# Optimization experiments

Measured on AMD Instinct MI355X. Metric: run time of the kernel, lower is better.

The kernel has to match this reference:

```python
import jax, jax.numpy as jnp
import numpy as np
import math

B, N, DIM = 2, 4096, 1024
H, D, M = 16, 64, 256


def setup_inputs() -> dict:
    key = jax.random.key(0)
    ks = jax.random.split(key, 6)
    s = 1.0 / math.sqrt(DIM)
    return {
        "x": jax.random.normal(ks[0], (B, N, DIM), dtype=jnp.float32),
        "w_q": jax.random.normal(ks[1], (DIM, H * D), dtype=jnp.float32) * s,
        "w_k": jax.random.normal(ks[2], (DIM, H * D), dtype=jnp.float32) * s,
        "w_v": jax.random.normal(ks[3], (DIM, H * D), dtype=jnp.float32) * s,
        "w_o": jax.random.normal(ks[4], (H * D, DIM), dtype=jnp.float32) * s,
        "b_o": jnp.zeros((DIM,), dtype=jnp.float32),
        "omega": jax.random.normal(ks[5], (M, D), dtype=jnp.float32),
    }


def _heads(t):
    # [B, N, H*D] -> [B, H, N, D]
    return t.reshape(B, N, H, D).transpose(0, 2, 1, 3)


def _phi(t, omega):
    # t: [B,H,N,D], omega: [M,D] -> [B,H,N,M]
    proj = jnp.einsum("bhnd,md->bhnm", t, omega)
    norm = 0.5 * jnp.sum(t * t, axis=-1, keepdims=True)
    return jnp.exp(proj - norm) / math.sqrt(M)


def reference(x, w_q, w_k, w_v, w_o, b_o, omega):
    q = _heads(x @ w_q)
    k = _heads(x @ w_k)
    v = _heads(x @ w_v)
    phi_q = _phi(q, omega)          # [B,H,N,M]
    phi_k = _phi(k, omega)          # [B,H,N,M]
    kv = jnp.einsum("bhnm,bhnd->bhmd", phi_k, v)   # [B,H,M,D]
    k_sum = phi_k.sum(axis=2)                       # [B,H,M]
    z = 1.0 / (jnp.einsum("bhnm,bhm->bhn", phi_q, k_sum) + 1e-6)
    out = jnp.einsum("bhnm,bhmd->bhnd", phi_q, kv) * z[..., None]
    out = out.transpose(0, 2, 1, 3).reshape(B, N, H * D)
    return out @ w_o + b_o
```

## Files before the change

kernel.cpp:

```cpp
#include <hip/hip_runtime.h>

#define DEVI __device__ __forceinline__

using f32x4 = __attribute__((ext_vector_type(4))) float;
using fvec4 = __attribute__((ext_vector_type(4))) float;
using s16x4 = __attribute__((ext_vector_type(4))) short;
using s16x8 = __attribute__((ext_vector_type(8))) short;

DEVI unsigned short f2bf_rn(float f) {
  union { float f; unsigned u; } v; v.f = f;
  unsigned r = v.u + 0x7fffu + ((v.u >> 16) & 1u);
  return (unsigned short)(r >> 16);
}
DEVI float bf2f(unsigned short h) {
  union { unsigned u; float f; } v; v.u = ((unsigned)h) << 16;
  return v.f;
}
DEVI f32x4 mfma16(s16x8 a, s16x8 b, f32x4 c) {
  return __builtin_amdgcn_mfma_f32_16x16x32_bf16(a, b, c, 0, 0, 0);
}
DEVI void gld16(const void* g, void* lds) {
  __builtin_amdgcn_global_load_lds(
      (const __attribute__((address_space(1))) unsigned int*)g,
      (__attribute__((address_space(3))) unsigned int*)lds, 16, 0, 0);
}

__global__ __launch_bounds__(256) void k_split_x(
    const float* __restrict__ X,
    unsigned short* __restrict__ XH, unsigned short* __restrict__ XL)
{
  size_t i = ((size_t)blockIdx.x * 256 + threadIdx.x) * 8;
  fvec4 a = *(const fvec4*)&X[i];
  fvec4 b = *(const fvec4*)&X[i + 4];
  s16x8 hv, lv;
#pragma unroll
  for (int j = 0; j < 4; ++j) {
    unsigned short h = f2bf_rn(a[j]);
    hv[j] = (short)h; lv[j] = (short)f2bf_rn(a[j] - bf2f(h));
  }
#pragma unroll
  for (int j = 0; j < 4; ++j) {
    unsigned short h = f2bf_rn(b[j]);
    hv[4 + j] = (short)h; lv[4 + j] = (short)f2bf_rn(b[j] - bf2f(h));
  }
  *(s16x8*)&XH[i] = hv;
  *(s16x8*)&XL[i] = lv;
}

__global__ __launch_bounds__(256) void k_prep_w(
    const float* __restrict__ wq, const float* __restrict__ wk,
    const float* __restrict__ wv, const float* __restrict__ wo,
    const float* __restrict__ omega,
    unsigned short* __restrict__ WTh, unsigned short* __restrict__ WOT,
    unsigned short* __restrict__ OMB)
{
  __shared__ float tile[64][65];
  const int z = blockIdx.z;
  const int t = threadIdx.x;
  if (z == 4) {
    int bid = blockIdx.x * 16 + blockIdx.y;
    if (bid < 16) {
      int i = (bid * 256 + t) * 4;
      fvec4 v = *(const fvec4*)&omega[i];
      s16x4 hv;
#pragma unroll
      for (int q = 0; q < 4; ++q) hv[q] = (short)f2bf_rn(v[q]);
      *(s16x4*)&OMB[i] = hv;
    }
    return;
  }
  const float* src = (z == 0) ? wq : (z == 1) ? wk : (z == 2) ? wv : wo;
  const int k0 = blockIdx.x * 64;
  const int n0 = blockIdx.y * 64;
#pragma unroll
  for (int j = 0; j < 4; ++j) {
    int r = (t >> 4) + 16 * j;
    int c = (t & 15) * 4;
    fvec4 v = *(const fvec4*)&src[(size_t)(k0 + r) * 1024 + n0 + c];
#pragma unroll
    for (int i = 0; i < 4; ++i) tile[r][c + i] = v[i];
  }
  __syncthreads();
#pragma unroll
  for (int j = 0; j < 4; ++j) {
    int n = (t >> 4) + 16 * j;
    int kc = (t & 15) * 4;
    s16x4 hv;
#pragma unroll
    for (int i = 0; i < 4; ++i) hv[i] = (short)f2bf_rn(tile[kc + i][n]);
    if (z < 3) {
      *(s16x4*)&WTh[(size_t)(z * 1024 + n0 + n) * 1024 + k0 + kc] = hv;
    } else {
      *(s16x4*)&WOT[(size_t)(n0 + n) * 1024 + k0 + kc] = hv;
    }
  }
}

__global__ __launch_bounds__(256) void k_gemm_qkv(
    const unsigned short* __restrict__ XH, const unsigned short* __restrict__ XL,
    const unsigned short* __restrict__ WTh,
    unsigned short* __restrict__ QH, unsigned short* __restrict__ QL,
    unsigned short* __restrict__ KH, unsigned short* __restrict__ KL,
    unsigned short* __restrict__ VB)
{
  __shared__ unsigned short AH[2][128 * 32];
  __shared__ unsigned short BHs[2][128 * 32];
  __shared__ unsigned short AL[2][128 * 32];
  const int flat = blockIdx.y * 24 + blockIdx.x;
  const int swz = (flat & 7) * 192 + (flat >> 3);
  const int cb = swz % 24;
  const int rb = swz / 24;
  const int t = threadIdx.x;
  const int w = t >> 6, l = t & 63;
  const bool tp = (cb < 16);
  f32x4 acc[4][4];
#pragma unroll
  for (int a = 0; a < 4; ++a)
#pragma unroll
    for (int b = 0; b < 4; ++b) acc[a][b] = (f32x4)0.f;

  const int r0 = w * 32;
  const int lrow = l >> 2;
  const int lcol = (l & 3) * 8;
  const size_t gA = (size_t)(rb * 128 + r0 + lrow) * 1024 + lcol;
  const size_t gB = (size_t)(cb * 128 + r0 + lrow) * 1024 + lcol;
  const int lds0 = r0 * 32;
  const int lds1 = (r0 + 16) * 32;

  const int wm = (w & 1) * 64, wn = (w >> 1) * 64;
  const int lr = l & 15, ko = (l >> 4) * 8;

  auto STAGE = [&](int buf, int k0) {
    gld16(&XH[gA + k0], &AH[buf][lds0]);
    gld16(&XH[gA + (size_t)16 * 1024 + k0], &AH[buf][lds1]);
    if (tp) {
      gld16(&XL[gA + k0], &AL[buf][lds0]);
      gld16(&XL[gA + (size_t)16 * 1024 + k0], &AL[buf][lds1]);
    }
    gld16(&WTh[gB + k0], &BHs[buf][lds0]);
    gld16(&WTh[gB + (size_t)16 * 1024 + k0], &BHs[buf][lds1]);
  };

  STAGE(0, 0);
  int cur = 0;
  for (int ks = 0; ks < 32; ++ks) {
    if (ks < 31) {
      STAGE(cur ^ 1, (ks + 1) * 32);
      if (tp) asm volatile("s_waitcnt vmcnt(6)" ::: "memory");
      else    asm volatile("s_waitcnt vmcnt(4)" ::: "memory");
    } else {
      asm volatile("s_waitcnt vmcnt(0)" ::: "memory");
    }
    __builtin_amdgcn_s_barrier();
    asm volatile("" ::: "memory");
    s16x8 ah[4], al[4], bh[4];
#pragma unroll
    for (int f = 0; f < 4; ++f) {
      ah[f] = *(const s16x8*)&AH[cur][(wm + f * 16 + lr) * 32 + ko];
      bh[f] = *(const s16x8*)&BHs[cur][(wn + f * 16 + lr) * 32 + ko];
    }
    if (tp) {
#pragma unroll
      for (int f = 0; f < 4; ++f) al[f] = *(const s16x8*)&AL[cur][(wm + f * 16 + lr) * 32 + ko];
    }
#pragma unroll
    for (int fa = 0; fa < 4; ++fa)
#pragma unroll
      for (int fb = 0; fb < 4; ++fb) {
        acc[fa][fb] = mfma16(ah[fa], bh[fb], acc[fa][fb]);
        if (tp) acc[fa][fb] = mfma16(al[fa], bh[fb], acc[fa][fb]);
      }
    asm volatile("s_waitcnt lgkmcnt(0)" ::: "memory");
    __builtin_amdgcn_s_barrier();
    asm volatile("" ::: "memory");
    cur ^= 1;
  }
  const int lg = l >> 4;
#pragma unroll
  for (int fa = 0; fa < 4; ++fa)
#pragma unroll
    for (int r = 0; r < 4; ++r) {
      int row = rb * 128 + wm + fa * 16 + lg * 4 + r;
#pragma unroll
      for (int fb = 0; fb < 4; ++fb) {
        int col = cb * 128 + wn + fb * 16 + lr;
        float v = acc[fa][fb][r];
        if (tp) {
          unsigned short hs = f2bf_rn(v);
          unsigned short ls = f2bf_rn(v - bf2f(hs));
          if (cb < 8) {
            QH[(size_t)row * 1024 + col] = hs;
            QL[(size_t)row * 1024 + col] = ls;
          } else {
            KH[(size_t)row * 1024 + col - 1024] = hs;
            KL[(size_t)row * 1024 + col - 1024] = ls;
          }
        } else {
          VB[(size_t)row * 1024 + col - 2048] = f2bf_rn(v);
        }
      }
    }
}

__global__ __launch_bounds__(512, 1) void k_phik_kv(
    const unsigned short* __restrict__ KH, const unsigned short* __restrict__ KL,
    const unsigned short* __restrict__ VB,
    const unsigned short* __restrict__ OMB, float* __restrict__ KVP)
{
  __shared__ unsigned short KHs[64][72], KLs[64][72];
  __shared__ unsigned short PKT[256][72];
  __shared__ unsigned short AVT[80][72];
  __shared__ float norm_s[64];
  const int nc = blockIdx.x;
  const int bh = blockIdx.y;
  const int b = bh >> 4, h = bh & 15;
  const int t = threadIdx.x, w = t >> 6, l = t & 63;
  const int lr = l & 15, lg = l >> 4, ko8 = lg * 8;

  s16x8 omf[2][2];
#pragma unroll
  for (int ksub = 0; ksub < 2; ++ksub)
#pragma unroll
    for (int f = 0; f < 2; ++f)
      omf[ksub][f] = *(const s16x8*)&OMB[(w * 32 + f * 16 + lr) * 64 + ksub * 32 + ko8];

  for (int e = t; e < 16 * 64; e += 512) {
    int rr = e >> 6, cc = e & 63;
    AVT[64 + rr][cc] = (rr == 0) ? (unsigned short)0x3F80 : (unsigned short)0;
  }

  f32x4 acc2[5][2];
#pragma unroll
  for (int a = 0; a < 5; ++a)
#pragma unroll
    for (int bb = 0; bb < 2; ++bb) acc2[a][bb] = (f32x4)0.f;

  for (int st = 0; st < 8; ++st) {
    const int n0 = nc * 512 + st * 64;
    __syncthreads();
    {
      int r = t >> 3, c8 = (t & 7) * 8;
      size_t o = (size_t)(b * 4096 + n0 + r) * 1024 + h * 64 + c8;
      s16x8 vh = *(const s16x8*)&KH[o];
      s16x8 vl = *(const s16x8*)&KL[o];
      *(s16x8*)&KHs[r][c8] = vh;
      *(s16x8*)&KLs[r][c8] = vl;
      float ss = 0.f;
#pragma unroll
      for (int i = 0; i < 8; ++i) {
        float q = bf2f((unsigned short)vh[i]) + bf2f((unsigned short)vl[i]);
        ss += q * q;
      }
      ss += __shfl_xor(ss, 1);
      ss += __shfl_xor(ss, 2);
      ss += __shfl_xor(ss, 4);
      if ((t & 7) == 0) norm_s[r] = 0.5f * ss;
    }
    {
      int n = t >> 3, dq = (t & 7) * 8;
      s16x8 v = *(const s16x8*)&VB[(size_t)(b * 4096 + n0 + n) * 1024 + h * 64 + dq];
#pragma unroll
      for (int i = 0; i < 8; ++i) AVT[dq + i][n] = (unsigned short)v[i];
    }
    __syncthreads();
    f32x4 acc[4][2];
#pragma unroll
    for (int a = 0; a < 4; ++a)
#pragma unroll
      for (int bb = 0; bb < 2; ++bb) acc[a][bb] = (f32x4)0.f;
#pragma unroll
    for (int ksub = 0; ksub < 2; ++ksub) {
      int ko = ksub * 32 + ko8;
      s16x8 ah[4], al[4];
#pragma unroll
      for (int f = 0; f < 4; ++f) {
        ah[f] = *(const s16x8*)&KHs[f * 16 + lr][ko];
        al[f] = *(const s16x8*)&KLs[f * 16 + lr][ko];
      }
#pragma unroll
      for (int fa = 0; fa < 4; ++fa)
#pragma unroll
        for (int fb = 0; fb < 2; ++fb) {
          acc[fa][fb] = mfma16(ah[fa], omf[ksub][fb], acc[fa][fb]);
          acc[fa][fb] = mfma16(al[fa], omf[ksub][fb], acc[fa][fb]);
        }
    }
#pragma unroll
    for (int fa = 0; fa < 4; ++fa)
#pragma unroll
      for (int r = 0; r < 4; ++r) {
        int n = fa * 16 + lg * 4 + r;
        float nm = norm_s[n];
#pragma unroll
        for (int fb = 0; fb < 2; ++fb) {
          int m = w * 32 + fb * 16 + lr;
          float p = __expf(acc[fa][fb][r] - nm) * 0.0625f;
          PKT[m][n] = f2bf_rn(p);
        }
      }
    __syncthreads();
#pragma unroll
    for (int ksub = 0; ksub < 2; ++ksub) {
      int ko = ksub * 32 + ko8;
      s16x8 fA[5], fB[2];
#pragma unroll
      for (int f = 0; f < 5; ++f) fA[f] = *(const s16x8*)&AVT[f * 16 + lr][ko];
#pragma unroll
      for (int f = 0; f < 2; ++f) fB[f] = *(const s16x8*)&PKT[w * 32 + f * 16 + lr][ko];
#pragma unroll
      for (int fa = 0; fa < 5; ++fa)
#pragma unroll
        for (int fb = 0; fb < 2; ++fb) acc2[fa][fb] = mfma16(fA[fa], fB[fb], acc2[fa][fb]);
    }
  }
#pragma unroll
  for (int fa = 0; fa < 5; ++fa)
#pragma unroll
    for (int r = 0; r < 4; ++r) {
      int dp = fa * 16 + lg * 4 + r;
#pragma unroll
      for (int fb = 0; fb < 2; ++fb) {
        int m = w * 32 + fb * 16 + lr;
        KVP[(size_t)((bh * 8 + nc) * 80 + dp) * 256 + m] = acc2[fa][fb][r];
      }
    }
}

__global__ __launch_bounds__(256) void k_kv_reduce(
    const float* __restrict__ KVP, unsigned short* __restrict__ KVTB)
{
  int idx = blockIdx.x * 256 + threadIdx.x;
  if (idx >= 32 * 80 * 256) return;
  int bh = idx / (80 * 256);
  int rem = idx % (80 * 256);
  float s = 0.f;
#pragma unroll
  for (int nci = 0; nci < 8; ++nci) s += KVP[(size_t)(bh * 8 + nci) * 80 * 256 + rem];
  KVTB[idx] = f2bf_rn(s);
}

__global__ __launch_bounds__(256) void k_phiq_attn(
    const unsigned short* QH, const unsigned short* QL,
    const unsigned short* __restrict__ OMB,
    const unsigned short* __restrict__ KVTB,
    unsigned short* ATT)
{
  __shared__ unsigned short QHs[64][72], QLs[64][72];
  __shared__ unsigned short PQ[64][264];
  __shared__ float norm_s[64];
  const int nt = blockIdx.x;
  const int bh = blockIdx.y;
  const int t = threadIdx.x, w = t >> 6, l = t & 63;
  const int b = bh >> 4, h = bh & 15;
  const int lr = l & 15, lg = l >> 4, ko8 = lg * 8;

  s16x8 omf[2][4];
#pragma unroll
  for (int ksub = 0; ksub < 2; ++ksub)
#pragma unroll
    for (int f = 0; f < 4; ++f)
      omf[ksub][f] = *(const s16x8*)&OMB[(w * 64 + f * 16 + lr) * 64 + ksub * 32 + ko8];

  {
    int r = t >> 2, cq = (t & 3) * 4;
    float ss = 0.f;
#pragma unroll
    for (int j = 0; j < 4; ++j) {
      int c = cq + 16 * j;
      size_t o = (size_t)(b * 4096 + nt * 64 + r) * 1024 + h * 64 + c;
      s16x4 vh = *(const s16x4*)&QH[o];
      s16x4 vl = *(const s16x4*)&QL[o];
      *(s16x4*)&QHs[r][c] = vh;
      *(s16x4*)&QLs[r][c] = vl;
#pragma unroll
      for (int i = 0; i < 4; ++i) {
        float q = bf2f((unsigned short)vh[i]) + bf2f((unsigned short)vl[i]);
        ss += q * q;
      }
    }
    ss += __shfl_xor(ss, 1);
    ss += __shfl_xor(ss, 2);
    if ((t & 3) == 0) norm_s[r] = 0.5f * ss;
  }
  __syncthreads();
  f32x4 acc[4][4];
#pragma unroll
  for (int a = 0; a < 4; ++a)
#pragma unroll
    for (int bb = 0; bb < 4; ++bb) acc[a][bb] = (f32x4)0.f;
#pragma unroll
  for (int ksub = 0; ksub < 2; ++ksub) {
    int ko = ksub * 32 + ko8;
    s16x8 ah[4], al[4];
#pragma unroll
    for (int f = 0; f < 4; ++f) {
      ah[f] = *(const s16x8*)&QHs[f * 16 + lr][ko];
      al[f] = *(const s16x8*)&QLs[f * 16 + lr][ko];
    }
#pragma unroll
    for (int fa = 0; fa < 4; ++fa)
#pragma unroll
      for (int fb = 0; fb < 4; ++fb) {
        acc[fa][fb] = mfma16(ah[fa], omf[ksub][fb], acc[fa][fb]);
        acc[fa][fb] = mfma16(al[fa], omf[ksub][fb], acc[fa][fb]);
      }
  }
#pragma unroll
  for (int fa = 0; fa < 4; ++fa)
#pragma unroll
    for (int r = 0; r < 4; ++r) {
      int n = fa * 16 + lg * 4 + r;
      float nm = norm_s[n];
#pragma unroll
      for (int fb = 0; fb < 4; ++fb) {
        int m = w * 64 + fb * 16 + lr;
        float p = __expf(acc[fa][fb][r] - nm) * 0.0625f;
        PQ[n][m] = f2bf_rn(p);
      }
    }
  __syncthreads();
  const size_t kvbase = (size_t)bh * 80 * 256;
  f32x4 acc2[5];
#pragma unroll
  for (int bb = 0; bb < 5; ++bb) acc2[bb] = (f32x4)0.f;
  for (int ks = 0; ks < 8; ++ks) {
    const int m0 = ks * 32;
    s16x8 fA = *(const s16x8*)&PQ[w * 16 + lr][m0 + ko8];
    s16x8 fB[5];
#pragma unroll
    for (int f = 0; f < 5; ++f)
      fB[f] = *(const s16x8*)&KVTB[kvbase + (size_t)(f * 16 + lr) * 256 + m0 + ko8];
#pragma unroll
    for (int fb = 0; fb < 5; ++fb) acc2[fb] = mfma16(fA, fB[fb], acc2[fb]);
  }
#pragma unroll
  for (int r = 0; r < 4; ++r) {
    float den = __shfl(acc2[4][r], (l & 48));
    float z = 1.f / (den + 1e-6f);
    int n = nt * 64 + w * 16 + lg * 4 + r;
#pragma unroll
    for (int fb = 0; fb < 4; ++fb) {
      int col = h * 64 + fb * 16 + lr;
      ATT[(size_t)(b * 4096 + n) * 1024 + col] = f2bf_rn(acc2[fb][r] * z);
    }
  }
}

__global__ __launch_bounds__(256) void k_gemm_out(
    const unsigned short* __restrict__ ATT,
    const unsigned short* __restrict__ WOT,
    const float* __restrict__ b_o,
    float* __restrict__ OUT)
{
  __shared__ unsigned short As[3][128 * 32], Bs[3][128 * 32];
  const int flat = blockIdx.y * 8 + blockIdx.x;
  const int swz = (flat & 7) * 64 + (flat >> 3);
  const int cb = swz % 8;
  const int rb = swz / 8;
  const int t = threadIdx.x, w = t >> 6, l = t & 63;
  f32x4 acc[4][4];
#pragma unroll
  for (int a = 0; a < 4; ++a)
#pragma unroll
    for (int bb = 0; bb < 4; ++bb) acc[a][bb] = (f32x4)0.f;

  const int r0 = w * 32;
  const int lrow = l >> 2;
  const int lcol = (l & 3) * 8;
  const size_t gA = (size_t)(rb * 128 + r0 + lrow) * 1024 + lcol;
  const size_t gB = (size_t)(cb * 128 + r0 + lrow) * 1024 + lcol;
  const int lds0 = r0 * 32;
  const int lds1 = (r0 + 16) * 32;

  const int wm = (w & 1) * 64, wn = (w >> 1) * 64;
  const int lr = l & 15, ko = (l >> 4) * 8;

  auto STAGE = [&](int buf, int k0) {
    gld16(&ATT[gA + k0], &As[buf][lds0]);
    gld16(&ATT[gA + (size_t)16 * 1024 + k0], &As[buf][lds1]);
    gld16(&WOT[gB + k0], &Bs[buf][lds0]);
    gld16(&WOT[gB + (size_t)16 * 1024 + k0], &Bs[buf][lds1]);
  };

  STAGE(0, 0);
  STAGE(1, 32);
  int cur = 0;
  for (int ks = 0; ks < 32; ++ks) {
    if (ks < 30) {
      int nxt = (cur >= 1) ? cur - 1 : 2;
      STAGE(nxt, (ks + 2) * 32);
      asm volatile("s_waitcnt vmcnt(8)" ::: "memory");
    } else if (ks == 30) {
      asm volatile("s_waitcnt vmcnt(4)" ::: "memory");
    } else {
      asm volatile("s_waitcnt vmcnt(0)" ::: "memory");
    }
    __builtin_amdgcn_s_barrier();
    asm volatile("" ::: "memory");
    s16x8 fA[4], fB[4];
#pragma unroll
    for (int f = 0; f < 4; ++f) {
      fA[f] = *(const s16x8*)&As[cur][(wm + f * 16 + lr) * 32 + ko];
      fB[f] = *(const s16x8*)&Bs[cur][(wn + f * 16 + lr) * 32 + ko];
    }
#pragma unroll
    for (int fa = 0; fa < 4; ++fa)
#pragma unroll
      for (int fb = 0; fb < 4; ++fb) acc[fa][fb] = mfma16(fA[fa], fB[fb], acc[fa][fb]);
    asm volatile("s_waitcnt lgkmcnt(0)" ::: "memory");
    __builtin_amdgcn_s_barrier();
    asm volatile("" ::: "memory");
    cur = (cur < 2) ? cur + 1 : 0;
  }
  const int lg = l >> 4;
#pragma unroll
  for (int fa = 0; fa < 4; ++fa)
#pragma unroll
    for (int r = 0; r < 4; ++r) {
      int row = rb * 128 + wm + fa * 16 + lg * 4 + r;
#pragma unroll
      for (int fb = 0; fb < 4; ++fb) {
        int col = cb * 128 + wn + fb * 16 + lr;
        OUT[(size_t)row * 1024 + col] = acc[fa][fb][r] + b_o[col];
      }
    }
}

extern "C" void kernel_launch(void* const* d_in, const int* in_sizes, int n_in,
                              void* d_out, int out_size, void* d_ws, size_t ws_size,
                              hipStream_t stream)
{
  const float* x  = (const float*)d_in[0];
  const float* wq = (const float*)d_in[1];
  const float* wk = (const float*)d_in[2];
  const float* wv = (const float*)d_in[3];
  const float* wo = (const float*)d_in[4];
  const float* bo = (const float*)d_in[5];
  const float* om = (const float*)d_in[6];
  float* out = (float*)d_out;

  const size_t PLANE = (size_t)8192 * 1024 * 2;
  char* ws = (char*)d_ws;
  unsigned short* WOT = (unsigned short*)(ws);
  char* segB = ws + 2097152;
  char* segC = segB + 2 * PLANE;
  char* segD = segC + 4 * PLANE;
  char* segE = segD + 26214400;

  unsigned short* QH  = (unsigned short*)segB;
  unsigned short* QL  = (unsigned short*)(segB + PLANE);
  unsigned short* ATT = (unsigned short*)segB;

  unsigned short* KH  = (unsigned short*)segC;
  unsigned short* KL  = (unsigned short*)(segC + PLANE);
  unsigned short* VB  = (unsigned short*)(segC + 2 * PLANE);
  unsigned short* XH  = (unsigned short*)(segC + 3 * PLANE);

  unsigned short* WTh = (unsigned short*)segD;
  unsigned short* XL  = (unsigned short*)(segD + 6291456);
  float* KVP = (float*)segD;
  unsigned short* KVTB = (unsigned short*)segE;
  unsigned short* OMB  = (unsigned short*)(segE + 1310720);

  k_split_x<<<dim3(4096), 256, 0, stream>>>(x, XH, XL);
  k_prep_w<<<dim3(16, 16, 5), 256, 0, stream>>>(wq, wk, wv, wo, om, WTh, WOT, OMB);
  k_gemm_qkv<<<dim3(24, 64), 256, 0, stream>>>(XH, XL, WTh, QH, QL, KH, KL, VB);
  k_phik_kv<<<dim3(8, 32), 512, 0, stream>>>(KH, KL, VB, OMB, KVP);
  k_kv_reduce<<<dim3(2560), 256, 0, stream>>>(KVP, KVTB);
  k_phiq_attn<<<dim3(64, 32), 256, 0, stream>>>(QH, QL, OMB, KVTB, ATT);
  k_gemm_out<<<dim3(8, 64), 256, 0, stream>>>(ATT, WOT, bo, out);
}
```

Before: 228.2 us.

## Load GEMM B fragments directly from global into registers, bypassing LDS

```diff
diff --git a/kernel.cpp b/kernel.cpp
--- a/kernel.cpp
+++ b/kernel.cpp
@@ -104,7 +104,6 @@
     unsigned short* __restrict__ VB)
 {
   __shared__ unsigned short AH[2][128 * 32];
-  __shared__ unsigned short BHs[2][128 * 32];
   __shared__ unsigned short AL[2][128 * 32];
   const int flat = blockIdx.y * 24 + blockIdx.x;
   const int swz = (flat & 7) * 192 + (flat >> 3);
@@ -123,12 +122,16 @@
   const int lrow = l >> 2;
   const int lcol = (l & 3) * 8;
   const size_t gA = (size_t)(rb * 128 + r0 + lrow) * 1024 + lcol;
-  const size_t gB = (size_t)(cb * 128 + r0 + lrow) * 1024 + lcol;
   const int lds0 = r0 * 32;
   const int lds1 = (r0 + 16) * 32;
 
   const int wm = (w & 1) * 64, wn = (w >> 1) * 64;
   const int lr = l & 15, ko = (l >> 4) * 8;
+
+  const unsigned short* Bp[4];
+#pragma unroll
+  for (int f = 0; f < 4; ++f)
+    Bp[f] = &WTh[(size_t)(cb * 128 + wn + f * 16 + lr) * 1024 + ko];
 
   auto STAGE = [&](int buf, int k0) {
     gld16(&XH[gA + k0], &AH[buf][lds0]);
@@ -137,32 +140,33 @@
       gld16(&XL[gA + k0], &AL[buf][lds0]);
       gld16(&XL[gA + (size_t)16 * 1024 + k0], &AL[buf][lds1]);
     }
-    gld16(&WTh[gB + k0], &BHs[buf][lds0]);
-    gld16(&WTh[gB + (size_t)16 * 1024 + k0], &BHs[buf][lds1]);
   };
 
   STAGE(0, 0);
   int cur = 0;
   for (int ks = 0; ks < 32; ++ks) {
+    const int k0 = ks * 32;
+    s16x8 bh[4];
+#pragma unroll
+    for (int f = 0; f < 4; ++f) bh[f] = *(const s16x8*)(Bp[f] + k0);
+    asm volatile("" ::: "memory");
     if (ks < 31) {
-      STAGE(cur ^ 1, (ks + 1) * 32);
-      if (tp) asm volatile("s_waitcnt vmcnt(6)" ::: "memory");
-      else    asm volatile("s_waitcnt vmcnt(4)" ::: "memory");
+      STAGE(cur ^ 1, k0 + 32);
+      if (tp) asm volatile("s_waitcnt vmcnt(8)" ::: "memory");
+      else    asm volatile("s_waitcnt vmcnt(6)" ::: "memory");
     } else {
-      asm volatile("s_waitcnt vmcnt(0)" ::: "memory");
+      asm volatile("s_waitcnt vmcnt(4)" ::: "memory");
     }
     __builtin_amdgcn_s_barrier();
     asm volatile("" ::: "memory");
-    s16x8 ah[4], al[4], bh[4];
-#pragma unroll
-    for (int f = 0; f < 4; ++f) {
-      ah[f] = *(const s16x8*)&AH[cur][(wm + f * 16 + lr) * 32 + ko];
-      bh[f] = *(const s16x8*)&BHs[cur][(wn + f * 16 + lr) * 32 + ko];
-    }
+    s16x8 ah[4], al[4];
+#pragma unroll
+    for (int f = 0; f < 4; ++f) ah[f] = *(const s16x8*)&AH[cur][(wm + f * 16 + lr) * 32 + ko];
     if (tp) {
 #pragma unroll
       for (int f = 0; f < 4; ++f) al[f] = *(const s16x8*)&AL[cur][(wm + f * 16 + lr) * 32 + ko];
     }
+    __builtin_amdgcn_s_setprio(1);
 #pragma unroll
     for (int fa = 0; fa < 4; ++fa)
 #pragma unroll
@@ -170,6 +174,7 @@
         acc[fa][fb] = mfma16(ah[fa], bh[fb], acc[fa][fb]);
         if (tp) acc[fa][fb] = mfma16(al[fa], bh[fb], acc[fa][fb]);
       }
+    __builtin_amdgcn_s_setprio(0);
     asm volatile("s_waitcnt lgkmcnt(0)" ::: "memory");
     __builtin_amdgcn_s_barrier();
     asm volatile("" ::: "memory");
@@ -452,7 +457,7 @@
     const float* __restrict__ b_o,
     float* __restrict__ OUT)
 {
-  __shared__ unsigned short As[3][128 * 32], Bs[3][128 * 32];
+  __shared__ unsigned short As[2][128 * 32];
   const int flat = blockIdx.y * 8 + blockIdx.x;
   const int swz = (flat & 7) * 64 + (flat >> 3);
   const int cb = swz % 8;
@@ -468,49 +473,51 @@
   const int lrow = l >> 2;
   const int lcol = (l & 3) * 8;
   const size_t gA = (size_t)(rb * 128 + r0 + lrow) * 1024 + lcol;
-  const size_t gB = (size_t)(cb * 128 + r0 + lrow) * 1024 + lcol;
   const int lds0 = r0 * 32;
   const int lds1 = (r0 + 16) * 32;
 
   const int wm = (w & 1) * 64, wn = (w >> 1) * 64;
   const int lr = l & 15, ko = (l >> 4) * 8;
+
+  const unsigned short* Bp[4];
+#pragma unroll
+  for (int f = 0; f < 4; ++f)
+    Bp[f] = &WOT[(size_t)(cb * 128 + wn + f * 16 + lr) * 1024 + ko];
 
   auto STAGE = [&](int buf, int k0) {
     gld16(&ATT[gA + k0], &As[buf][lds0]);
     gld16(&ATT[gA + (size_t)16 * 1024 + k0], &As[buf][lds1]);
-    gld16(&WOT[gB + k0], &Bs[buf][lds0]);
-    gld16(&WOT[gB + (size_t)16 * 1024 + k0], &Bs[buf][lds1]);
   };
 
   STAGE(0, 0);
-  STAGE(1, 32);
   int cur = 0;
   for (int ks = 0; ks < 32; ++ks) {
-    if (ks < 30) {
-      int nxt = (cur >= 1) ? cur - 1 : 2;
-      STAGE(nxt, (ks + 2) * 32);
-      asm volatile("s_waitcnt vmcnt(8)" ::: "memory");
-    } else if (ks == 30) {
+    const int k0 = ks * 32;
+    s16x8 fB[4];
+#pragma unroll
+    for (int f = 0; f < 4; ++f) fB[f] = *(const s16x8*)(Bp[f] + k0);
+    asm volatile("" ::: "memory");
+    if (ks < 31) {
+      STAGE(cur ^ 1, k0 + 32);
+      asm volatile("s_waitcnt vmcnt(6)" ::: "memory");
+    } else {
       asm volatile("s_waitcnt vmcnt(4)" ::: "memory");
-    } else {
-      asm volatile("s_waitcnt vmcnt(0)" ::: "memory");
     }
     __builtin_amdgcn_s_barrier();
     asm volatile("" ::: "memory");
-    s16x8 fA[4], fB[4];
-#pragma unroll
-    for (int f = 0; f < 4; ++f) {
-      fA[f] = *(const s16x8*)&As[cur][(wm + f * 16 + lr) * 32 + ko];
-      fB[f] = *(const s16x8*)&Bs[cur][(wn + f * 16 + lr) * 32 + ko];
-    }
+    s16x8 fA[4];
+#pragma unroll
+    for (int f = 0; f < 4; ++f) fA[f] = *(const s16x8*)&As[cur][(wm + f * 16 + lr) * 32 + ko];
+    __builtin_amdgcn_s_setprio(1);
 #pragma unroll
     for (int fa = 0; fa < 4; ++fa)
 #pragma unroll
       for (int fb = 0; fb < 4; ++fb) acc[fa][fb] = mfma16(fA[fa], fB[fb], acc[fa][fb]);
+    __builtin_amdgcn_s_setprio(0);
     asm volatile("s_waitcnt lgkmcnt(0)" ::: "memory");
     __builtin_amdgcn_s_barrier();
     asm volatile("" ::: "memory");
-    cur = (cur < 2) ? cur + 1 : 0;
+    cur ^= 1;
   }
   const int lg = l >> 4;
 #pragma unroll
```

After: 288.0 us. 1.26x slower.
